# Optimization experiments

Hardware: AMD Instinct MI355X
Metric: run time of the kernel (lower is better)

## Reference

```python
import jax, jax.numpy as jnp
import numpy as np

N = 768                       # atoms
E = N * (N - 1)               # complete directed graph edges
DIM = 64                      # hidden dim
CUT = 5.0                     # rbf high
NC = 50                       # n_centers = ceil(5/0.1)
ODIM = 1                      # output_dim
NCONV = 3
_centers_np = np.linspace(0.0, CUT, NC)
CENTERS = jnp.asarray(_centers_np, jnp.float32)
GAP = float(_centers_np[1] - _centers_np[0])
RO_IN = 2 * ODIM + NC         # readout input: 2*output_dim + rbf fan_out = 52


def softplus_bt(x, beta, thr):
    # torch.nn.Softplus(beta, threshold): linear above threshold
    bx = beta * x
    return jnp.where(bx > thr, x, jax.nn.softplus(bx) / beta)


def rbf(d):
    # exp(-(1/gap) * (d - mu_k)^2); d: (..., 1) -> (..., NC)
    return jnp.exp((-1.0 / GAP) * (d - CENTERS) ** 2)


def setup_inputs() -> dict:
    key = jax.random.key(0)
    ks = jax.random.split(key, 24)
    atom_types = jax.random.randint(ks[0], (N,), 0, 100)
    edge_distances = jax.random.uniform(ks[1], (E, 1), jnp.float32) * CUT
    # complete directed graph, edge order matches the nested i,j loop (i!=j)
    ii = np.repeat(np.arange(N), N)
    jj = np.tile(np.arange(N), N)
    m = ii != jj
    src = jnp.asarray(ii[m], jnp.int32)
    dst = jnp.asarray(jj[m], jnp.int32)

    def p(k, shape, fan):
        return jax.random.normal(k, shape, jnp.float32) / np.sqrt(fan)

    embedding = p(ks[2], (100, DIM), DIM).at[0].set(0.0)  # padding_idx=0
    L = NCONV
    return {
        'atom_types': atom_types, 'edge_distances': edge_distances,
        'src': src, 'dst': dst, 'embedding': embedding,
        'w1': p(ks[3], (L, DIM, DIM), DIM),                 # node_layer1 (no bias)
        'pw1': p(ks[4], (L, NC, DIM), NC), 'pb1': p(ks[5], (L, DIM), NC),
        'pw2': p(ks[6], (L, DIM, DIM), DIM), 'pb2': p(ks[7], (L, DIM), DIM),
        'qw1': p(ks[8], (L, DIM, DIM), DIM), 'qb1': p(ks[9], (L, DIM), DIM),
        'qw2': p(ks[10], (L, DIM, DIM), DIM), 'qb2': p(ks[11], (L, DIM), DIM),
        'au_w1': p(ks[12], (DIM, 64), DIM), 'au_b1': p(ks[13], (64,), DIM),
        'au_w2': p(ks[14], (64, ODIM), 64), 'au_b2': p(ks[15], (ODIM,), 64),
        'ro_w1': p(ks[16], (RO_IN, 64), RO_IN), 'ro_b1': p(ks[17], (64,), RO_IN),
        'ro_w2': p(ks[18], (64, 2), 64), 'ro_b2': p(ks[19], (2,), 64),
    }


def reference(atom_types, edge_distances, src, dst, embedding,
              w1, pw1, pb1, pw2, pb2, qw1, qb1, qw2, qb2,
              au_w1, au_b1, au_w2, au_b2, ro_w1, ro_b1, ro_w2, ro_b2):
    h = embedding[atom_types]                       # (N, DIM)
    rbf_out = rbf(edge_distances)                   # (E, NC)
    for l in range(NCONV):
        nw = h @ w1[l]                              # node weights (N, DIM)
        e = softplus_bt(rbf_out @ pw1[l] + pb1[l], 0.5, 14) @ pw2[l] + pb2[l]  # (E, DIM)
        msg = nw[src] * e                           # gather-mul (E, DIM)
        agg = jax.ops.segment_sum(msg, dst, num_segments=N)  # scatter-sum (N, DIM)
        upd = softplus_bt(agg @ qw1[l] + qb1[l], 0.5, 14) @ qw2[l] + qb2[l]
        h = h + upd
    # atom_update with ShiftSoftplus (beta=1, shift=2, threshold=20)
    ha = softplus_bt(h @ au_w1 + au_b1, 1.0, 20) - jnp.log(jnp.float32(2.0))
    ha = ha @ au_w2 + au_b2                         # (N, ODIM)
    # readout over all ordered pairs i!=j, in edge order == (src, dst)
    edge_feat = jnp.concatenate([ha[src], ha[dst], rbf_out], axis=-1)  # (E, 52)
    logits = jax.nn.relu(edge_feat @ ro_w1 + ro_b1) @ ro_w2 + ro_b2    # (E, 2)
    return jax.nn.softmax(logits, axis=-1)
```

## Files before the change

kernel.cpp:

```cpp
#include <hip/hip_runtime.h>
#include <hip/hip_fp16.h>

#define NATOMS 768
#define NM1    767
#define NEDGE  (768*767)
#define DIM    64
#define NC     50
#define GAPF   (5.0f/49.0f)
#define NIGAP  (-49.0f/5.0f)
#define G      512
#define STEPF  (5.0f/511.0f)
#define INVSTEP (511.0f/5.0f)
#define LN2F   0.693147180559945f

#define WS_H     0
#define WS_NWA   49152
#define WS_NWB   73728
#define WS_HA    98304
#define WS_DISTT 99328
#define WS_TT    689152

__device__ __forceinline__ float softplus05(float x) {
    float bx = 0.5f * x;
    return (bx > 14.0f) ? x : 2.0f * __logf(1.0f + __expf(bx));
}
__device__ __forceinline__ int lane_bcast_i(int v, int l) {
    return __builtin_amdgcn_readlane(v, l);
}
__device__ __forceinline__ float lane_bcast_f(float v, int l) {
    return __uint_as_float((unsigned)__builtin_amdgcn_readlane((int)__float_as_uint(v), l));
}
__device__ __forceinline__ float2 pair2f(unsigned p) {
    __half2 h = *reinterpret_cast<__half2*>(&p);
    return __half22float2(h);
}

__global__ __launch_bounds__(256)
void k_pre(const int* __restrict__ types, const float* __restrict__ dist,
           const float* __restrict__ emb, const float* __restrict__ w1all,
           const float* __restrict__ pw1, const float* __restrict__ pb1,
           const float* __restrict__ pw2, const float* __restrict__ pb2,
           const float* __restrict__ row1, const float* __restrict__ rob1,
           float* __restrict__ ws) {
    __shared__ float s_t[4 * 64];
    __shared__ float s_tile[64][65];
    const int tid = threadIdx.x, widx = tid >> 6, c = tid & 63;
    float*  h     = ws + WS_H;
    __half* nwh   = (__half*)(ws + WS_NWA);
    float*  distT = ws + WS_DISTT;
    __half* TTh   = (__half*)(ws + WS_TT);
    const int b = blockIdx.x;

    if (b < 512) {
        const int w = b * 4 + widx, tbl = w >> 9, g = w & 511;
        const float d = g * STEPF;
        float val;
        if (tbl < 3) {
            const float* W1 = pw1 + tbl * NC * DIM;
            float t1 = pb1[tbl * DIM + c];
            for (int k = 0; k < NC; ++k) {
                float x = d - GAPF * (float)k;
                t1 = fmaf(__expf(NIGAP * x * x), W1[k * DIM + c], t1);
            }
            s_t[widx * 64 + c] = softplus05(t1);
            const float* W2 = pw2 + tbl * DIM * DIM;
            val = pb2[tbl * DIM + c];
            #pragma unroll 8
            for (int k = 0; k < DIM; ++k)
                val = fmaf(s_t[widx * 64 + k], W2[k * DIM + c], val);
        } else {
            val = rob1[c];
            for (int k = 0; k < NC; ++k) {
                float x = d - GAPF * (float)k;
                val = fmaf(__expf(NIGAP * x * x), row1[(2 + k) * DIM + c], val);
            }
        }
        __half* TTt = TTh + tbl * (G * DIM * 2);
        TTt[(g * DIM + c) * 2] = __float2half(val);
        if (g > 0) TTt[((g - 1) * DIM + c) * 2 + 1] = __float2half(val);
    } else if (b < 704) {
        const int i = (b - 512) * 4 + widx;
        float hv = emb[types[i] * DIM + c];
        h[i * DIM + c] = hv;
        s_t[widx * 64 + c] = hv;
        float acc = 0.0f;
        #pragma unroll 8
        for (int k = 0; k < DIM; ++k)
            acc = fmaf(s_t[widx * 64 + k], w1all[k * DIM + c], acc);
        nwh[(i >> 1) * 128 + c * 2 + (i & 1)] = __float2half(acc);
    } else {
        const int t = b - 704;
        const int I0 = (t / 12) * 64, J0 = (t % 12) * 64;
        #pragma unroll 4
        for (int r = 0; r < 16; ++r) {
            const int i = I0 + widx * 16 + r;
            const int j = J0 + c;
            s_tile[widx * 16 + r][c] =
                (i == j) ? 0.0f : dist[i * NM1 + (j - (j > i))];
        }
        __syncthreads();
        #pragma unroll 4
        for (int r = 0; r < 16; ++r) {
            const int j = J0 + widx * 16 + r;
            const int i = I0 + c;
            distT[j * NATOMS + i] = s_tile[c][widx * 16 + r];
        }
    }
}

__global__ __launch_bounds__(512)
void k_edgeupd(const __half2* __restrict__ TTl, const float* __restrict__ distT,
               const __half2* __restrict__ nwin,
               const float* __restrict__ qw1, const float* __restrict__ qb1,
               const float* __restrict__ qw2, const float* __restrict__ qb2,
               float* __restrict__ h,
               const float* __restrict__ wnext, __half* __restrict__ nwout,
               const float* __restrict__ auw1, const float* __restrict__ aub1,
               const float* __restrict__ auw2, const float* __restrict__ aub2,
               float* __restrict__ ha, int last) {
    __shared__ float s_part[8][64];
    __shared__ float s_upd[192];
    const int tid = threadIdx.x, widx = tid >> 6, c = tid & 63;
    const int j = blockIdx.x;
    const int s0 = widx * 96;

    const char* TTb = (const char*)TTl + c * 4;
    float csum = 0.0f;
    {
        float d = distT[j * NATOMS + s0 + c];
        float pos = d * INVSTEP;
        int g = (int)pos;
        g = (g < 0) ? 0 : ((g > 510) ? 510 : g);
        float f = pos - (float)g;
        int kx = g * 256;
        const char* nwrow = (const char*)(nwin + (s0 >> 1) * 64 + c);
        for (int grp = 0; grp < 4; ++grp) {
            unsigned sa[8], sb[8], sn[8];
            #pragma unroll
            for (int u = 0; u < 8; ++u) {
                const int t = grp * 8 + u;
                int kx0 = lane_bcast_i(kx, 2 * t);
                int kx1 = lane_bcast_i(kx, 2 * t + 1);
                sa[u] = *(const unsigned*)(TTb + kx0);
                sb[u] = *(const unsigned*)(TTb + kx1);
                sn[u] = *(const unsigned*)(nwrow + t * 256);
            }
            #pragma unroll
            for (int u = 0; u < 8; ++u) {
                const int t = grp * 8 + u;
                float f0 = lane_bcast_f(f, 2 * t);
                float f1 = lane_bcast_f(f, 2 * t + 1);
                float2 ta = pair2f(sa[u]);
                float2 tb = pair2f(sb[u]);
                float2 nwf = pair2f(sn[u]);
                float e0 = fmaf(f0, ta.y - ta.x, ta.x);
                float e1 = fmaf(f1, tb.y - tb.x, tb.x);
                csum = fmaf(e0, nwf.x, csum);
                csum = fmaf(e1, nwf.y, csum);
            }
        }
    }
    {
        float d = distT[j * NATOMS + s0 + 64 + (c & 31)];
        float pos = d * INVSTEP;
        int g = (int)pos;
        g = (g < 0) ? 0 : ((g > 510) ? 510 : g);
        float f = pos - (float)g;
        int kx = g * 256;
        const char* nwrow = (const char*)(nwin + ((s0 + 64) >> 1) * 64 + c);
        for (int grp = 0; grp < 2; ++grp) {
            unsigned sa[8], sb[8], sn[8];
            #pragma unroll
            for (int u = 0; u < 8; ++u) {
                const int t = grp * 8 + u;
                int kx0 = lane_bcast_i(kx, 2 * t);
                int kx1 = lane_bcast_i(kx, 2 * t + 1);
                sa[u] = *(const unsigned*)(TTb + kx0);
                sb[u] = *(const unsigned*)(TTb + kx1);
                sn[u] = *(const unsigned*)(nwrow + t * 256);
            }
            #pragma unroll
            for (int u = 0; u < 8; ++u) {
                const int t = grp * 8 + u;
                float f0 = lane_bcast_f(f, 2 * t);
                float f1 = lane_bcast_f(f, 2 * t + 1);
                float2 ta = pair2f(sa[u]);
                float2 tb = pair2f(sb[u]);
                float2 nwf = pair2f(sn[u]);
                float e0 = fmaf(f0, ta.y - ta.x, ta.x);
                float e1 = fmaf(f1, tb.y - tb.x, tb.x);
                csum = fmaf(e0, nwf.x, csum);
                csum = fmaf(e1, nwf.y, csum);
            }
        }
    }
    s_part[widx][c] = csum;
    __syncthreads();

    if (widx == 0) {
        float tot = 0.0f;
        #pragma unroll
        for (int w8 = 0; w8 < 8; ++w8) tot += s_part[w8][c];
        float2 t0 = __half22float2(*(const __half2*)TTb);
        float nwj = __half2float(((const __half*)nwin)[(j >> 1) * 128 + c * 2 + (j & 1)]);
        tot -= t0.x * nwj;
        s_upd[c] = tot;
        float t = qb1[c];
        #pragma unroll 8
        for (int k = 0; k < DIM; ++k) t = fmaf(s_upd[k], qw1[k * DIM + c], t);
        s_upd[64 + c] = softplus05(t);
        float o = qb2[c];
        #pragma unroll 8
        for (int k = 0; k < DIM; ++k) o = fmaf(s_upd[64 + k], qw2[k * DIM + c], o);
        float hn = h[j * DIM + c] + o;
        h[j * DIM + c] = hn;
        s_upd[128 + c] = hn;
        if (!last) {
            float v = 0.0f;
            #pragma unroll 8
            for (int k = 0; k < DIM; ++k) v = fmaf(s_upd[128 + k], wnext[k * DIM + c], v);
            nwout[(j >> 1) * 128 + c * 2 + (j & 1)] = __float2half(v);
        } else {
            float t2 = aub1[c];
            #pragma unroll 8
            for (int k = 0; k < DIM; ++k) t2 = fmaf(s_upd[128 + k], auw1[k * DIM + c], t2);
            t2 = ((t2 > 20.0f) ? t2 : __logf(1.0f + __expf(t2))) - LN2F;
            float v = t2 * auw2[c];
            #pragma unroll
            for (int s = 32; s > 0; s >>= 1) v += __shfl_down(v, s, 64);
            if (c == 0) ha[j] = v + aub2[0];
        }
    }
}

__global__ __launch_bounds__(256)
void k_ro(const float* __restrict__ dist, const int* __restrict__ src,
          const int* __restrict__ dst, const float* __restrict__ ha,
          const __half2* __restrict__ TTro,
          const float* __restrict__ row1, const float* __restrict__ row2,
          const float* __restrict__ rob2, float* __restrict__ out) {
    __shared__ float s_h[4][16 * 65];
    __shared__ float s_w2[128];
    const int tid = threadIdx.x, widx = tid >> 6, c = tid & 63;
    if (tid < 128) s_w2[tid] = row2[tid];
    __syncthreads();
    const int ebase = (blockIdx.x * 4 + widx) * 64;

    int kxv; float ff, fa, fb;
    {
        int eg = ebase + c;
        float d = dist[eg];
        float pos = d * INVSTEP;
        int kk = (int)pos;
        kk = (kk < 0) ? 0 : ((kk > 510) ? 510 : kk);
        kxv = kk * 256;
        ff = pos - (float)kk;
        fa = ha[src[eg]];
        fb = ha[dst[eg]];
    }
    const char* TTb2 = (const char*)TTro + c * 4;
    const float wa = row1[c], wb = row1[DIM + c];
    const int e2 = (c >> 1) & 15, p2 = c & 1, kh = c >> 5;
    const float bias2 = (kh == 0) ? rob2[p2] : 0.0f;
    float* sh = s_h[widx];
    #pragma unroll
    for (int ch = 0; ch < 4; ++ch) {
        #pragma unroll
        for (int half = 0; half < 2; ++half) {
            unsigned st[8];
            #pragma unroll
            for (int u = 0; u < 8; ++u) {
                const int le = ch * 16 + half * 8 + u;
                int kxu = lane_bcast_i(kxv, le);
                st[u] = *(const unsigned*)(TTb2 + kxu);
            }
            #pragma unroll
            for (int u = 0; u < 8; ++u) {
                const int le = ch * 16 + half * 8 + u;
                const int e = half * 8 + u;
                float fu  = lane_bcast_f(ff, le);
                float fau = lane_bcast_f(fa, le);
                float fbu = lane_bcast_f(fb, le);
                float2 tt = pair2f(st[u]);
                float hv = fmaf(fu, tt.y - tt.x, tt.x);
                hv = fmaf(fau, wa, hv);
                hv = fmaf(fbu, wb, hv);
                sh[e * 65 + c] = fmaxf(hv, 0.0f);
            }
        }
        float lsum = bias2;
        #pragma unroll 8
        for (int k8 = 0; k8 < 32; ++k8) {
            int k = kh * 32 + k8;
            lsum = fmaf(sh[e2 * 65 + k], s_w2[2 * k + p2], lsum);
        }
        lsum += __shfl_xor(lsum, 32, 64);
        float other = __shfl_xor(lsum, 1, 64);
        float m = fmaxf(lsum, other);
        float ea = __expf(lsum - m), eb = __expf(other - m);
        float r = ea / (ea + eb);
        if (c < 32) out[ebase * 2 + ch * 32 + c] = r;
    }
}

extern "C" void kernel_launch(void* const* d_in, const int* in_sizes, int n_in,
                              void* d_out, int out_size, void* d_ws, size_t ws_size,
                              hipStream_t stream) {
    const int*   types = (const int*)d_in[0];
    const float* dist  = (const float*)d_in[1];
    const int*   srcI  = (const int*)d_in[2];
    const int*   dstI  = (const int*)d_in[3];
    const float* emb   = (const float*)d_in[4];
    const float* w1    = (const float*)d_in[5];
    const float* pw1   = (const float*)d_in[6];
    const float* pb1   = (const float*)d_in[7];
    const float* pw2   = (const float*)d_in[8];
    const float* pb2   = (const float*)d_in[9];
    const float* qw1   = (const float*)d_in[10];
    const float* qb1   = (const float*)d_in[11];
    const float* qw2   = (const float*)d_in[12];
    const float* qb2   = (const float*)d_in[13];
    const float* auw1  = (const float*)d_in[14];
    const float* aub1  = (const float*)d_in[15];
    const float* auw2  = (const float*)d_in[16];
    const float* aub2  = (const float*)d_in[17];
    const float* row1  = (const float*)d_in[18];
    const float* rob1  = (const float*)d_in[19];
    const float* row2  = (const float*)d_in[20];
    const float* rob2  = (const float*)d_in[21];

    float* ws   = (float*)d_ws;
    float* outp = (float*)d_out;
    const __half2* TT = (const __half2*)(ws + WS_TT);
    __half2* nwbuf[2] = { (__half2*)(ws + WS_NWA), (__half2*)(ws + WS_NWB) };

    k_pre<<<848, 256, 0, stream>>>(types, dist, emb, w1, pw1, pb1, pw2, pb2,
                                   row1, rob1, ws);
    for (int l = 0; l < 3; ++l) {
        k_edgeupd<<<768, 512, 0, stream>>>(TT + l * (G * DIM),
            ws + WS_DISTT, nwbuf[l & 1],
            qw1 + l * DIM * DIM, qb1 + l * DIM,
            qw2 + l * DIM * DIM, qb2 + l * DIM,
            ws + WS_H,
            (l < 2) ? (w1 + (l + 1) * DIM * DIM) : w1, (__half*)nwbuf[(l + 1) & 1],
            auw1, aub1, auw2, aub2, ws + WS_HA, (l == 2) ? 1 : 0);
    }
    k_ro<<<2301, 256, 0, stream>>>(dist, srcI, dstI, ws + WS_HA, TT + 3 * (G * DIM),
                                   row1, row2, rob2, outp);
}
```

Baseline: 182.3 us.

## Fuse preprocessing and conv layers into one persistent kernel with grid barriers

Merges the preprocessing kernel and the three per-layer edge-update kernels into a single 768-block kernel, separated by a hierarchical atomic grid barrier in place of kernel launch boundaries. The distance transpose is rewritten as a plain strided copy instead of a shared-memory tiled transpose. The readout kernel now computes the src/dst atom indices arithmetically from the edge id instead of loading them from the index arrays. The aim is to cut launch overhead and tail gaps between the four kernels. In exchange it depends on all 768 blocks being co-resident, which the launch-bounds hint of six blocks per CU is meant to allow, and it adds a memset launch to reset the barrier.

```diff
diff --git a/kernel.cpp b/kernel.cpp
--- a/kernel.cpp
+++ b/kernel.cpp
@@ -19,6 +19,7 @@
 #define WS_HA    98304
 #define WS_DISTT 99328
 #define WS_TT    689152
+#define WS_BAR   820224
 
 __device__ __forceinline__ float softplus05(float x) {
     float bx = 0.5f * x;
@@ -35,207 +36,233 @@
     return __half22float2(h);
 }
 
-__global__ __launch_bounds__(256)
-void k_pre(const int* __restrict__ types, const float* __restrict__ dist,
-           const float* __restrict__ emb, const float* __restrict__ w1all,
+__device__ __forceinline__ void gbar(int* bar, int blk) {
+    __syncthreads();
+    if (threadIdx.x == 0) {
+        __threadfence();
+        int* root = bar;
+        int* gen  = bar + 16;
+        int* l1   = bar + 32 + (blk & 63) * 16;
+        int g = __hip_atomic_load(gen, __ATOMIC_RELAXED, __HIP_MEMORY_SCOPE_AGENT);
+        int a = __hip_atomic_fetch_add(l1, 1, __ATOMIC_ACQ_REL, __HIP_MEMORY_SCOPE_AGENT);
+        if (a == 11) {
+            __hip_atomic_store(l1, 0, __ATOMIC_RELAXED, __HIP_MEMORY_SCOPE_AGENT);
+            int r = __hip_atomic_fetch_add(root, 1, __ATOMIC_ACQ_REL, __HIP_MEMORY_SCOPE_AGENT);
+            if (r == 63) {
+                __hip_atomic_store(root, 0, __ATOMIC_RELAXED, __HIP_MEMORY_SCOPE_AGENT);
+                __hip_atomic_fetch_add(gen, 1, __ATOMIC_RELEASE, __HIP_MEMORY_SCOPE_AGENT);
+            } else {
+                while (__hip_atomic_load(gen, __ATOMIC_ACQUIRE, __HIP_MEMORY_SCOPE_AGENT) == g)
+                    __builtin_amdgcn_s_sleep(2);
+            }
+        } else {
+            while (__hip_atomic_load(gen, __ATOMIC_ACQUIRE, __HIP_MEMORY_SCOPE_AGENT) == g)
+                __builtin_amdgcn_s_sleep(2);
+        }
+        __threadfence();
+    }
+    __syncthreads();
+}
+
+__global__ __launch_bounds__(512, 6)
+void k_net(const int* __restrict__ types, const float* __restrict__ dist,
+           const float* __restrict__ emb, const float* __restrict__ w1,
            const float* __restrict__ pw1, const float* __restrict__ pb1,
            const float* __restrict__ pw2, const float* __restrict__ pb2,
+           const float* __restrict__ qw1, const float* __restrict__ qb1,
+           const float* __restrict__ qw2, const float* __restrict__ qb2,
+           const float* __restrict__ auw1, const float* __restrict__ aub1,
+           const float* __restrict__ auw2, const float* __restrict__ aub2,
            const float* __restrict__ row1, const float* __restrict__ rob1,
            float* __restrict__ ws) {
-    __shared__ float s_t[4 * 64];
-    __shared__ float s_tile[64][65];
-    const int tid = threadIdx.x, widx = tid >> 6, c = tid & 63;
-    float*  h     = ws + WS_H;
-    __half* nwh   = (__half*)(ws + WS_NWA);
-    float*  distT = ws + WS_DISTT;
-    __half* TTh   = (__half*)(ws + WS_TT);
-    const int b = blockIdx.x;
-
-    if (b < 512) {
-        const int w = b * 4 + widx, tbl = w >> 9, g = w & 511;
-        const float d = g * STEPF;
-        float val;
-        if (tbl < 3) {
-            const float* W1 = pw1 + tbl * NC * DIM;
-            float t1 = pb1[tbl * DIM + c];
-            for (int k = 0; k < NC; ++k) {
-                float x = d - GAPF * (float)k;
-                t1 = fmaf(__expf(NIGAP * x * x), W1[k * DIM + c], t1);
-            }
-            s_t[widx * 64 + c] = softplus05(t1);
-            const float* W2 = pw2 + tbl * DIM * DIM;
-            val = pb2[tbl * DIM + c];
-            #pragma unroll 8
-            for (int k = 0; k < DIM; ++k)
-                val = fmaf(s_t[widx * 64 + k], W2[k * DIM + c], val);
-        } else {
-            val = rob1[c];
-            for (int k = 0; k < NC; ++k) {
-                float x = d - GAPF * (float)k;
-                val = fmaf(__expf(NIGAP * x * x), row1[(2 + k) * DIM + c], val);
-            }
-        }
-        __half* TTt = TTh + tbl * (G * DIM * 2);
-        TTt[(g * DIM + c) * 2] = __float2half(val);
-        if (g > 0) TTt[((g - 1) * DIM + c) * 2 + 1] = __float2half(val);
-    } else if (b < 704) {
-        const int i = (b - 512) * 4 + widx;
-        float hv = emb[types[i] * DIM + c];
-        h[i * DIM + c] = hv;
-        s_t[widx * 64 + c] = hv;
-        float acc = 0.0f;
-        #pragma unroll 8
-        for (int k = 0; k < DIM; ++k)
-            acc = fmaf(s_t[widx * 64 + k], w1all[k * DIM + c], acc);
-        nwh[(i >> 1) * 128 + c * 2 + (i & 1)] = __float2half(acc);
-    } else {
-        const int t = b - 704;
-        const int I0 = (t / 12) * 64, J0 = (t % 12) * 64;
-        #pragma unroll 4
-        for (int r = 0; r < 16; ++r) {
-            const int i = I0 + widx * 16 + r;
-            const int j = J0 + c;
-            s_tile[widx * 16 + r][c] =
-                (i == j) ? 0.0f : dist[i * NM1 + (j - (j > i))];
-        }
-        __syncthreads();
-        #pragma unroll 4
-        for (int r = 0; r < 16; ++r) {
-            const int j = J0 + widx * 16 + r;
-            const int i = I0 + c;
-            distT[j * NATOMS + i] = s_tile[c][widx * 16 + r];
-        }
-    }
-}
-
-__global__ __launch_bounds__(512)
-void k_edgeupd(const __half2* __restrict__ TTl, const float* __restrict__ distT,
-               const __half2* __restrict__ nwin,
-               const float* __restrict__ qw1, const float* __restrict__ qb1,
-               const float* __restrict__ qw2, const float* __restrict__ qb2,
-               float* __restrict__ h,
-               const float* __restrict__ wnext, __half* __restrict__ nwout,
-               const float* __restrict__ auw1, const float* __restrict__ aub1,
-               const float* __restrict__ auw2, const float* __restrict__ aub2,
-               float* __restrict__ ha, int last) {
+    __shared__ float s_t[8][64];
     __shared__ float s_part[8][64];
     __shared__ float s_upd[192];
     const int tid = threadIdx.x, widx = tid >> 6, c = tid & 63;
-    const int j = blockIdx.x;
+    const int blk = blockIdx.x;
+    int* bar = (int*)(ws + WS_BAR);
+
+    float*   h     = ws + WS_H;
+    float*   haV   = ws + WS_HA;
+    float*   distT = ws + WS_DISTT;
+    __half*  TTh   = (__half*)(ws + WS_TT);
+    const __half2* TT = (const __half2*)(ws + WS_TT);
+    __half2* nwb[2] = { (__half2*)(ws + WS_NWA), (__half2*)(ws + WS_NWB) };
+
+    {
+        const int W = blk * 8 + widx;
+        if (W < 2048) {
+            const int tbl = W >> 9, g = W & 511;
+            const float d = g * STEPF;
+            float val;
+            if (tbl < 3) {
+                const float* W1 = pw1 + tbl * NC * DIM;
+                float t1 = pb1[tbl * DIM + c];
+                for (int k = 0; k < NC; ++k) {
+                    float x = d - GAPF * (float)k;
+                    t1 = fmaf(__expf(NIGAP * x * x), W1[k * DIM + c], t1);
+                }
+                s_t[widx][c] = softplus05(t1);
+                const float* W2 = pw2 + tbl * DIM * DIM;
+                val = pb2[tbl * DIM + c];
+                #pragma unroll 8
+                for (int k = 0; k < DIM; ++k)
+                    val = fmaf(s_t[widx][k], W2[k * DIM + c], val);
+            } else {
+                val = rob1[c];
+                for (int k = 0; k < NC; ++k) {
+                    float x = d - GAPF * (float)k;
+                    val = fmaf(__expf(NIGAP * x * x), row1[(2 + k) * DIM + c], val);
+                }
+            }
+            __half* TTt = TTh + tbl * (G * DIM * 2);
+            TTt[(g * DIM + c) * 2] = __float2half(val);
+            if (g > 0) TTt[((g - 1) * DIM + c) * 2 + 1] = __float2half(val);
+        } else if (W < 2816) {
+            const int i = W - 2048;
+            float hv = emb[types[i] * DIM + c];
+            h[i * DIM + c] = hv;
+            s_t[widx][c] = hv;
+            float acc = 0.0f;
+            #pragma unroll 8
+            for (int k = 0; k < DIM; ++k)
+                acc = fmaf(s_t[widx][k], w1[k * DIM + c], acc);
+            ((__half*)nwb[0])[(i >> 1) * 128 + c * 2 + (i & 1)] = __float2half(acc);
+        } else if (W < 3392) {
+            const int u = W - 2816;
+            for (int t = 0; t < 16; ++t) {
+                const int idx = u * 1024 + t * 64 + c;
+                const int jj = idx / NATOMS, ii = idx - jj * NATOMS;
+                distT[idx] = (ii == jj) ? 0.0f : dist[ii * NM1 + (jj - (jj > ii))];
+            }
+        }
+    }
+    gbar(bar, blk);
+
+    const int j = blk;
     const int s0 = widx * 96;
-
-    const char* TTb = (const char*)TTl + c * 4;
-    float csum = 0.0f;
-    {
-        float d = distT[j * NATOMS + s0 + c];
-        float pos = d * INVSTEP;
-        int g = (int)pos;
-        g = (g < 0) ? 0 : ((g > 510) ? 510 : g);
-        float f = pos - (float)g;
-        int kx = g * 256;
-        const char* nwrow = (const char*)(nwin + (s0 >> 1) * 64 + c);
-        for (int grp = 0; grp < 4; ++grp) {
-            unsigned sa[8], sb[8], sn[8];
+    for (int l = 0; l < 3; ++l) {
+        const __half2* TTl   = TT + l * (G * DIM);
+        const __half2* nwin  = nwb[l & 1];
+        __half*        nwout = (__half*)nwb[(l + 1) & 1];
+        const float* qw1l = qw1 + l * DIM * DIM; const float* qb1l = qb1 + l * DIM;
+        const float* qw2l = qw2 + l * DIM * DIM; const float* qb2l = qb2 + l * DIM;
+        const float* wnx  = (l < 2) ? (w1 + (l + 1) * DIM * DIM) : w1;
+        const int last = (l == 2);
+
+        const char* TTb = (const char*)TTl + c * 4;
+        float csum = 0.0f;
+        {
+            float d = distT[j * NATOMS + s0 + c];
+            float pos = d * INVSTEP;
+            int g = (int)pos;
+            g = (g < 0) ? 0 : ((g > 510) ? 510 : g);
+            float f = pos - (float)g;
+            int kx = g * 256;
+            const char* nwrow = (const char*)(nwin + (s0 >> 1) * 64 + c);
+            for (int grp = 0; grp < 4; ++grp) {
+                unsigned sa[8], sb[8], sn[8];
+                #pragma unroll
+                for (int u = 0; u < 8; ++u) {
+                    const int t = grp * 8 + u;
+                    int kx0 = lane_bcast_i(kx, 2 * t);
+                    int kx1 = lane_bcast_i(kx, 2 * t + 1);
+                    sa[u] = *(const unsigned*)(TTb + kx0);
+                    sb[u] = *(const unsigned*)(TTb + kx1);
+                    sn[u] = *(const unsigned*)(nwrow + t * 256);
+                }
+                #pragma unroll
+                for (int u = 0; u < 8; ++u) {
+                    const int t = grp * 8 + u;
+                    float f0 = lane_bcast_f(f, 2 * t);
+                    float f1 = lane_bcast_f(f, 2 * t + 1);
+                    float2 ta = pair2f(sa[u]);
+                    float2 tb = pair2f(sb[u]);
+                    float2 nwf = pair2f(sn[u]);
+                    float e0 = fmaf(f0, ta.y - ta.x, ta.x);
+                    float e1 = fmaf(f1, tb.y - tb.x, tb.x);
+                    csum = fmaf(e0, nwf.x, csum);
+                    csum = fmaf(e1, nwf.y, csum);
+                }
+            }
+        }
+        {
+            float d = distT[j * NATOMS + s0 + 64 + (c & 31)];
+            float pos = d * INVSTEP;
+            int g = (int)pos;
+            g = (g < 0) ? 0 : ((g > 510) ? 510 : g);
+            float f = pos - (float)g;
+            int kx = g * 256;
+            const char* nwrow = (const char*)(nwin + ((s0 + 64) >> 1) * 64 + c);
+            for (int grp = 0; grp < 2; ++grp) {
+                unsigned sa[8], sb[8], sn[8];
+                #pragma unroll
+                for (int u = 0; u < 8; ++u) {
+                    const int t = grp * 8 + u;
+                    int kx0 = lane_bcast_i(kx, 2 * t);
+                    int kx1 = lane_bcast_i(kx, 2 * t + 1);
+                    sa[u] = *(const unsigned*)(TTb + kx0);
+                    sb[u] = *(const unsigned*)(TTb + kx1);
+                    sn[u] = *(const unsigned*)(nwrow + t * 256);
+                }
+                #pragma unroll
+                for (int u = 0; u < 8; ++u) {
+                    const int t = grp * 8 + u;
+                    float f0 = lane_bcast_f(f, 2 * t);
+                    float f1 = lane_bcast_f(f, 2 * t + 1);
+                    float2 ta = pair2f(sa[u]);
+                    float2 tb = pair2f(sb[u]);
+                    float2 nwf = pair2f(sn[u]);
+                    float e0 = fmaf(f0, ta.y - ta.x, ta.x);
+                    float e1 = fmaf(f1, tb.y - tb.x, tb.x);
+                    csum = fmaf(e0, nwf.x, csum);
+                    csum = fmaf(e1, nwf.y, csum);
+                }
+            }
+        }
+        s_part[widx][c] = csum;
+        __syncthreads();
+
+        if (widx == 0) {
+            float tot = 0.0f;
             #pragma unroll
-            for (int u = 0; u < 8; ++u) {
-                const int t = grp * 8 + u;
-                int kx0 = lane_bcast_i(kx, 2 * t);
-                int kx1 = lane_bcast_i(kx, 2 * t + 1);
-                sa[u] = *(const unsigned*)(TTb + kx0);
-                sb[u] = *(const unsigned*)(TTb + kx1);
-                sn[u] = *(const unsigned*)(nwrow + t * 256);
-            }
-            #pragma unroll
-            for (int u = 0; u < 8; ++u) {
-                const int t = grp * 8 + u;
-                float f0 = lane_bcast_f(f, 2 * t);
-                float f1 = lane_bcast_f(f, 2 * t + 1);
-                float2 ta = pair2f(sa[u]);
-                float2 tb = pair2f(sb[u]);
-                float2 nwf = pair2f(sn[u]);
-                float e0 = fmaf(f0, ta.y - ta.x, ta.x);
-                float e1 = fmaf(f1, tb.y - tb.x, tb.x);
-                csum = fmaf(e0, nwf.x, csum);
-                csum = fmaf(e1, nwf.y, csum);
-            }
-        }
-    }
-    {
-        float d = distT[j * NATOMS + s0 + 64 + (c & 31)];
-        float pos = d * INVSTEP;
-        int g = (int)pos;
-        g = (g < 0) ? 0 : ((g > 510) ? 510 : g);
-        float f = pos - (float)g;
-        int kx = g * 256;
-        const char* nwrow = (const char*)(nwin + ((s0 + 64) >> 1) * 64 + c);
-        for (int grp = 0; grp < 2; ++grp) {
-            unsigned sa[8], sb[8], sn[8];
-            #pragma unroll
-            for (int u = 0; u < 8; ++u) {
-                const int t = grp * 8 + u;
-                int kx0 = lane_bcast_i(kx, 2 * t);
-                int kx1 = lane_bcast_i(kx, 2 * t + 1);
-                sa[u] = *(const unsigned*)(TTb + kx0);
-                sb[u] = *(const unsigned*)(TTb + kx1);
-                sn[u] = *(const unsigned*)(nwrow + t * 256);
-            }
-            #pragma unroll
-            for (int u = 0; u < 8; ++u) {
-                const int t = grp * 8 + u;
-                float f0 = lane_bcast_f(f, 2 * t);
-                float f1 = lane_bcast_f(f, 2 * t + 1);
-                float2 ta = pair2f(sa[u]);
-                float2 tb = pair2f(sb[u]);
-                float2 nwf = pair2f(sn[u]);
-                float e0 = fmaf(f0, ta.y - ta.x, ta.x);
-                float e1 = fmaf(f1, tb.y - tb.x, tb.x);
-                csum = fmaf(e0, nwf.x, csum);
-                csum = fmaf(e1, nwf.y, csum);
-            }
-        }
-    }
-    s_part[widx][c] = csum;
-    __syncthreads();
-
-    if (widx == 0) {
-        float tot = 0.0f;
-        #pragma unroll
-        for (int w8 = 0; w8 < 8; ++w8) tot += s_part[w8][c];
-        float2 t0 = __half22float2(*(const __half2*)TTb);
-        float nwj = __half2float(((const __half*)nwin)[(j >> 1) * 128 + c * 2 + (j & 1)]);
-        tot -= t0.x * nwj;
-        s_upd[c] = tot;
-        float t = qb1[c];
-        #pragma unroll 8
-        for (int k = 0; k < DIM; ++k) t = fmaf(s_upd[k], qw1[k * DIM + c], t);
-        s_upd[64 + c] = softplus05(t);
-        float o = qb2[c];
-        #pragma unroll 8
-        for (int k = 0; k < DIM; ++k) o = fmaf(s_upd[64 + k], qw2[k * DIM + c], o);
-        float hn = h[j * DIM + c] + o;
-        h[j * DIM + c] = hn;
-        s_upd[128 + c] = hn;
-        if (!last) {
-            float v = 0.0f;
+            for (int w8 = 0; w8 < 8; ++w8) tot += s_part[w8][c];
+            float2 t0 = __half22float2(*(const __half2*)TTb);
+            float nwj = __half2float(((const __half*)nwin)[(j >> 1) * 128 + c * 2 + (j & 1)]);
+            tot -= t0.x * nwj;
+            s_upd[c] = tot;
+            float t = qb1l[c];
             #pragma unroll 8
-            for (int k = 0; k < DIM; ++k) v = fmaf(s_upd[128 + k], wnext[k * DIM + c], v);
-            nwout[(j >> 1) * 128 + c * 2 + (j & 1)] = __float2half(v);
-        } else {
-            float t2 = aub1[c];
+            for (int k = 0; k < DIM; ++k) t = fmaf(s_upd[k], qw1l[k * DIM + c], t);
+            s_upd[64 + c] = softplus05(t);
+            float o = qb2l[c];
             #pragma unroll 8
-            for (int k = 0; k < DIM; ++k) t2 = fmaf(s_upd[128 + k], auw1[k * DIM + c], t2);
-            t2 = ((t2 > 20.0f) ? t2 : __logf(1.0f + __expf(t2))) - LN2F;
-            float v = t2 * auw2[c];
-            #pragma unroll
-            for (int s = 32; s > 0; s >>= 1) v += __shfl_down(v, s, 64);
-            if (c == 0) ha[j] = v + aub2[0];
-        }
+            for (int k = 0; k < DIM; ++k) o = fmaf(s_upd[64 + k], qw2l[k * DIM + c], o);
+            float hn = h[j * DIM + c] + o;
+            h[j * DIM + c] = hn;
+            s_upd[128 + c] = hn;
+            if (!last) {
+                float v = 0.0f;
+                #pragma unroll 8
+                for (int k = 0; k < DIM; ++k) v = fmaf(s_upd[128 + k], wnx[k * DIM + c], v);
+                nwout[(j >> 1) * 128 + c * 2 + (j & 1)] = __float2half(v);
+            } else {
+                float t2 = aub1[c];
+                #pragma unroll 8
+                for (int k = 0; k < DIM; ++k) t2 = fmaf(s_upd[128 + k], auw1[k * DIM + c], t2);
+                t2 = ((t2 > 20.0f) ? t2 : __logf(1.0f + __expf(t2))) - LN2F;
+                float v = t2 * auw2[c];
+                #pragma unroll
+                for (int s = 32; s > 0; s >>= 1) v += __shfl_down(v, s, 64);
+                if (c == 0) haV[j] = v + aub2[0];
+            }
+        }
+        if (!last) gbar(bar, blk);
     }
 }
 
 __global__ __launch_bounds__(256)
-void k_ro(const float* __restrict__ dist, const int* __restrict__ src,
-          const int* __restrict__ dst, const float* __restrict__ ha,
+void k_ro(const float* __restrict__ dist, const float* __restrict__ ha,
           const __half2* __restrict__ TTro,
           const float* __restrict__ row1, const float* __restrict__ row2,
           const float* __restrict__ rob2, float* __restrict__ out) {
@@ -255,8 +282,11 @@
         kk = (kk < 0) ? 0 : ((kk > 510) ? 510 : kk);
         kxv = kk * 256;
         ff = pos - (float)kk;
-        fa = ha[src[eg]];
-        fb = ha[dst[eg]];
+        unsigned i = (unsigned)(((unsigned long long)(unsigned)eg * 2867044662ull) >> 41);
+        int r = eg - (int)i * 767;
+        int jd = r + (r >= (int)i);
+        fa = ha[i];
+        fb = ha[jd];
     }
     const char* TTb2 = (const char*)TTro + c * 4;
     const float wa = row1[c], wb = row1[DIM + c];
@@ -308,8 +338,6 @@
                               hipStream_t stream) {
     const int*   types = (const int*)d_in[0];
     const float* dist  = (const float*)d_in[1];
-    const int*   srcI  = (const int*)d_in[2];
-    const int*   dstI  = (const int*)d_in[3];
     const float* emb   = (const float*)d_in[4];
     const float* w1    = (const float*)d_in[5];
     const float* pw1   = (const float*)d_in[6];
@@ -332,19 +360,11 @@
     float* ws   = (float*)d_ws;
     float* outp = (float*)d_out;
     const __half2* TT = (const __half2*)(ws + WS_TT);
-    __half2* nwbuf[2] = { (__half2*)(ws + WS_NWA), (__half2*)(ws + WS_NWB) };
-
-    k_pre<<<848, 256, 0, stream>>>(types, dist, emb, w1, pw1, pb1, pw2, pb2,
+
+    hipMemsetAsync(ws + WS_BAR, 0, 1056 * sizeof(int), stream);
+    k_net<<<768, 512, 0, stream>>>(types, dist, emb, w1, pw1, pb1, pw2, pb2,
+                                   qw1, qb1, qw2, qb2, auw1, aub1, auw2, aub2,
                                    row1, rob1, ws);
-    for (int l = 0; l < 3; ++l) {
-        k_edgeupd<<<768, 512, 0, stream>>>(TT + l * (G * DIM),
-            ws + WS_DISTT, nwbuf[l & 1],
-            qw1 + l * DIM * DIM, qb1 + l * DIM,
-            qw2 + l * DIM * DIM, qb2 + l * DIM,
-            ws + WS_H,
-            (l < 2) ? (w1 + (l + 1) * DIM * DIM) : w1, (__half*)nwbuf[(l + 1) & 1],
-            auw1, aub1, auw2, aub2, ws + WS_HA, (l == 2) ? 1 : 0);
-    }
-    k_ro<<<2301, 256, 0, stream>>>(dist, srcI, dstI, ws + WS_HA, TT + 3 * (G * DIM),
+    k_ro<<<2301, 256, 0, stream>>>(dist, ws + WS_HA, TT + 3 * (G * DIM),
                                    row1, row2, rob2, outp);
 }
```

Measured after the change: 639.5 us. 251% more time.

## Split conv aggregation across three blocks per atom with last-block reduction

Applied to the files above, without the earlier changes.

The per-atom aggregation kernel now runs three 256-thread blocks per destination atom instead of one 512-thread block. Each block writes a partial sum to a workspace buffer, and an atomic counter picks the last block to finish the reduction and the node MLP. This raises grid size and occupancy, and removes the odd half-wave tail segment. Separately, the readout kernel derives the src/dst indices arithmetically from the edge index instead of loading the index arrays. The cost is extra global traffic, threadfences, atomics and a memset per launch.

```diff
diff --git a/kernel.cpp b/kernel.cpp
--- a/kernel.cpp
+++ b/kernel.cpp
@@ -19,6 +19,8 @@
 #define WS_HA    98304
 #define WS_DISTT 99328
 #define WS_TT    689152
+#define WS_PART  820224
+#define WS_CNT   967680
 
 __device__ __forceinline__ float softplus05(float x) {
     float bx = 0.5f * x;
@@ -108,42 +110,45 @@
     }
 }
 
-__global__ __launch_bounds__(512)
-void k_edgeupd(const __half2* __restrict__ TTl, const float* __restrict__ distT,
-               const __half2* __restrict__ nwin,
-               const float* __restrict__ qw1, const float* __restrict__ qb1,
-               const float* __restrict__ qw2, const float* __restrict__ qb2,
-               float* __restrict__ h,
-               const float* __restrict__ wnext, __half* __restrict__ nwout,
-               const float* __restrict__ auw1, const float* __restrict__ aub1,
-               const float* __restrict__ auw2, const float* __restrict__ aub2,
-               float* __restrict__ ha, int last) {
-    __shared__ float s_part[8][64];
+__global__ __launch_bounds__(256, 8)
+void k_conv(const __half2* __restrict__ TTl, const float* __restrict__ distT,
+            const __half2* __restrict__ nwin,
+            const float* __restrict__ qw1, const float* __restrict__ qb1,
+            const float* __restrict__ qw2, const float* __restrict__ qb2,
+            float* __restrict__ h,
+            const float* __restrict__ wnext, __half* __restrict__ nwout,
+            const float* __restrict__ auw1, const float* __restrict__ aub1,
+            const float* __restrict__ auw2, const float* __restrict__ aub2,
+            float* __restrict__ ha, float* __restrict__ pbuf, int* __restrict__ cnt,
+            int last) {
+    __shared__ float s_part[4][64];
     __shared__ float s_upd[192];
+    __shared__ int s_flag;
     const int tid = threadIdx.x, widx = tid >> 6, c = tid & 63;
-    const int j = blockIdx.x;
-    const int s0 = widx * 96;
+    const int b = blockIdx.x;
+    const int j = b / 3, seg = b - j * 3;
+    const int sb = seg * 256 + widx * 64;
 
     const char* TTb = (const char*)TTl + c * 4;
     float csum = 0.0f;
     {
-        float d = distT[j * NATOMS + s0 + c];
+        float d = distT[j * NATOMS + sb + c];
         float pos = d * INVSTEP;
         int g = (int)pos;
         g = (g < 0) ? 0 : ((g > 510) ? 510 : g);
         float f = pos - (float)g;
         int kx = g * 256;
-        const char* nwrow = (const char*)(nwin + (s0 >> 1) * 64 + c);
+        const char* nwrow = (const char*)(nwin + (sb >> 1) * 64 + c);
         for (int grp = 0; grp < 4; ++grp) {
-            unsigned sa[8], sb[8], sn[8];
+            unsigned sa[8], sb8[8], sn[8];
             #pragma unroll
             for (int u = 0; u < 8; ++u) {
                 const int t = grp * 8 + u;
                 int kx0 = lane_bcast_i(kx, 2 * t);
                 int kx1 = lane_bcast_i(kx, 2 * t + 1);
-                sa[u] = *(const unsigned*)(TTb + kx0);
-                sb[u] = *(const unsigned*)(TTb + kx1);
-                sn[u] = *(const unsigned*)(nwrow + t * 256);
+                sa[u]  = *(const unsigned*)(TTb + kx0);
+                sb8[u] = *(const unsigned*)(TTb + kx1);
+                sn[u]  = *(const unsigned*)(nwrow + t * 256);
             }
             #pragma unroll
             for (int u = 0; u < 8; ++u) {
@@ -151,7 +156,7 @@
                 float f0 = lane_bcast_f(f, 2 * t);
                 float f1 = lane_bcast_f(f, 2 * t + 1);
                 float2 ta = pair2f(sa[u]);
-                float2 tb = pair2f(sb[u]);
+                float2 tb = pair2f(sb8[u]);
                 float2 nwf = pair2f(sn[u]);
                 float e0 = fmaf(f0, ta.y - ta.x, ta.x);
                 float e1 = fmaf(f1, tb.y - tb.x, tb.x);
@@ -160,47 +165,27 @@
             }
         }
     }
-    {
-        float d = distT[j * NATOMS + s0 + 64 + (c & 31)];
-        float pos = d * INVSTEP;
-        int g = (int)pos;
-        g = (g < 0) ? 0 : ((g > 510) ? 510 : g);
-        float f = pos - (float)g;
-        int kx = g * 256;
-        const char* nwrow = (const char*)(nwin + ((s0 + 64) >> 1) * 64 + c);
-        for (int grp = 0; grp < 2; ++grp) {
-            unsigned sa[8], sb[8], sn[8];
-            #pragma unroll
-            for (int u = 0; u < 8; ++u) {
-                const int t = grp * 8 + u;
-                int kx0 = lane_bcast_i(kx, 2 * t);
-                int kx1 = lane_bcast_i(kx, 2 * t + 1);
-                sa[u] = *(const unsigned*)(TTb + kx0);
-                sb[u] = *(const unsigned*)(TTb + kx1);
-                sn[u] = *(const unsigned*)(nwrow + t * 256);
-            }
-            #pragma unroll
-            for (int u = 0; u < 8; ++u) {
-                const int t = grp * 8 + u;
-                float f0 = lane_bcast_f(f, 2 * t);
-                float f1 = lane_bcast_f(f, 2 * t + 1);
-                float2 ta = pair2f(sa[u]);
-                float2 tb = pair2f(sb[u]);
-                float2 nwf = pair2f(sn[u]);
-                float e0 = fmaf(f0, ta.y - ta.x, ta.x);
-                float e1 = fmaf(f1, tb.y - tb.x, tb.x);
-                csum = fmaf(e0, nwf.x, csum);
-                csum = fmaf(e1, nwf.y, csum);
-            }
-        }
-    }
     s_part[widx][c] = csum;
     __syncthreads();
 
     if (widx == 0) {
-        float tot = 0.0f;
-        #pragma unroll
-        for (int w8 = 0; w8 < 8; ++w8) tot += s_part[w8][c];
+        float p = s_part[0][c] + s_part[1][c] + s_part[2][c] + s_part[3][c];
+        pbuf[(j * 3 + seg) * 64 + c] = p;
+        __threadfence();
+    }
+    __syncthreads();
+    if (tid == 0) {
+        int old = atomicAdd(&cnt[j], 1);
+        s_flag = (old == 2);
+    }
+    __syncthreads();
+    if (!s_flag) return;
+
+    if (widx == 0) {
+        __threadfence();
+        float tot = pbuf[(j * 3 + 0) * 64 + c]
+                  + pbuf[(j * 3 + 1) * 64 + c]
+                  + pbuf[(j * 3 + 2) * 64 + c];
         float2 t0 = __half22float2(*(const __half2*)TTb);
         float nwj = __half2float(((const __half*)nwin)[(j >> 1) * 128 + c * 2 + (j & 1)]);
         tot -= t0.x * nwj;
@@ -230,12 +215,12 @@
             for (int s = 32; s > 0; s >>= 1) v += __shfl_down(v, s, 64);
             if (c == 0) ha[j] = v + aub2[0];
         }
+        if (c == 0) cnt[j] = 0;
     }
 }
 
 __global__ __launch_bounds__(256)
-void k_ro(const float* __restrict__ dist, const int* __restrict__ src,
-          const int* __restrict__ dst, const float* __restrict__ ha,
+void k_ro(const float* __restrict__ dist, const float* __restrict__ ha,
           const __half2* __restrict__ TTro,
           const float* __restrict__ row1, const float* __restrict__ row2,
           const float* __restrict__ rob2, float* __restrict__ out) {
@@ -255,8 +240,11 @@
         kk = (kk < 0) ? 0 : ((kk > 510) ? 510 : kk);
         kxv = kk * 256;
         ff = pos - (float)kk;
-        fa = ha[src[eg]];
-        fb = ha[dst[eg]];
+        unsigned i = (unsigned)(((unsigned long long)(unsigned)eg * 2867044662ull) >> 41);
+        int r = eg - (int)i * 767;
+        int jd = r + (r >= (int)i);
+        fa = ha[i];
+        fb = ha[jd];
     }
     const char* TTb2 = (const char*)TTro + c * 4;
     const float wa = row1[c], wb = row1[DIM + c];
@@ -308,8 +296,6 @@
                               hipStream_t stream) {
     const int*   types = (const int*)d_in[0];
     const float* dist  = (const float*)d_in[1];
-    const int*   srcI  = (const int*)d_in[2];
-    const int*   dstI  = (const int*)d_in[3];
     const float* emb   = (const float*)d_in[4];
     const float* w1    = (const float*)d_in[5];
     const float* pw1   = (const float*)d_in[6];
@@ -333,18 +319,21 @@
     float* outp = (float*)d_out;
     const __half2* TT = (const __half2*)(ws + WS_TT);
     __half2* nwbuf[2] = { (__half2*)(ws + WS_NWA), (__half2*)(ws + WS_NWB) };
-
+    float* pbuf = ws + WS_PART;
+    int*   cnt  = (int*)(ws + WS_CNT);
+
+    hipMemsetAsync(cnt, 0, 768 * sizeof(int), stream);
     k_pre<<<848, 256, 0, stream>>>(types, dist, emb, w1, pw1, pb1, pw2, pb2,
                                    row1, rob1, ws);
     for (int l = 0; l < 3; ++l) {
-        k_edgeupd<<<768, 512, 0, stream>>>(TT + l * (G * DIM),
+        k_conv<<<2304, 256, 0, stream>>>(TT + l * (G * DIM),
             ws + WS_DISTT, nwbuf[l & 1],
             qw1 + l * DIM * DIM, qb1 + l * DIM,
             qw2 + l * DIM * DIM, qb2 + l * DIM,
             ws + WS_H,
             (l < 2) ? (w1 + (l + 1) * DIM * DIM) : w1, (__half*)nwbuf[(l + 1) & 1],
-            auw1, aub1, auw2, aub2, ws + WS_HA, (l == 2) ? 1 : 0);
-    }
-    k_ro<<<2301, 256, 0, stream>>>(dist, srcI, dstI, ws + WS_HA, TT + 3 * (G * DIM),
+            auw1, aub1, auw2, aub2, ws + WS_HA, pbuf, cnt, (l == 2) ? 1 : 0);
+    }
+    k_ro<<<2301, 256, 0, stream>>>(dist, ws + WS_HA, TT + 3 * (G * DIM),
                                    row1, row2, rob2, outp);
 }
```

Measured after the change: 397.9 us. 118% more time.

## Split lanes across source halves with 8-byte table loads; compute src/dst analytically

Applied to the files above, without the earlier changes.

The node-weight buffer becomes a plain row-major half array. In the edge-update kernel, each half-wavefront now handles one of the two interleaved sources, using a single 8-byte table load that covers two channels instead of two 4-byte loads. The two halves are combined with a cross-lane shuffle before the shared-memory reduction. The readout kernel stops loading src/dst indices and derives them from the edge id with a magic-number division, which relies on the fixed complete-graph edge ordering.

```diff
diff --git a/kernel.cpp b/kernel.cpp
--- a/kernel.cpp
+++ b/kernel.cpp
@@ -87,7 +87,7 @@
         #pragma unroll 8
         for (int k = 0; k < DIM; ++k)
             acc = fmaf(s_t[widx * 64 + k], w1all[k * DIM + c], acc);
-        nwh[(i >> 1) * 128 + c * 2 + (i & 1)] = __float2half(acc);
+        nwh[i * 64 + c] = __float2half(acc);
     } else {
         const int t = b - 704;
         const int I0 = (t / 12) * 64, J0 = (t % 12) * 64;
@@ -110,7 +110,7 @@
 
 __global__ __launch_bounds__(512)
 void k_edgeupd(const __half2* __restrict__ TTl, const float* __restrict__ distT,
-               const __half2* __restrict__ nwin,
+               const __half* __restrict__ nwin,
                const float* __restrict__ qw1, const float* __restrict__ qb1,
                const float* __restrict__ qw2, const float* __restrict__ qb2,
                float* __restrict__ h,
@@ -123,9 +123,10 @@
     const int tid = threadIdx.x, widx = tid >> 6, c = tid & 63;
     const int j = blockIdx.x;
     const int s0 = widx * 96;
-
-    const char* TTb = (const char*)TTl + c * 4;
-    float csum = 0.0f;
+    const int half = c >> 5, cl = c & 31;
+
+    const char* TTrow = (const char*)TTl + cl * 8;
+    float2 csum = make_float2(0.0f, 0.0f);
     {
         float d = distT[j * NATOMS + s0 + c];
         float pos = d * INVSTEP;
@@ -133,16 +134,16 @@
         g = (g < 0) ? 0 : ((g > 510) ? 510 : g);
         float f = pos - (float)g;
         int kx = g * 256;
-        const char* nwrow = (const char*)(nwin + (s0 >> 1) * 64 + c);
+        const char* nwrow = (const char*)nwin + s0 * 128 + half * 128 + cl * 4;
         for (int grp = 0; grp < 4; ++grp) {
-            unsigned sa[8], sb[8], sn[8];
+            uint2 st[8]; unsigned sn[8];
             #pragma unroll
             for (int u = 0; u < 8; ++u) {
                 const int t = grp * 8 + u;
                 int kx0 = lane_bcast_i(kx, 2 * t);
                 int kx1 = lane_bcast_i(kx, 2 * t + 1);
-                sa[u] = *(const unsigned*)(TTb + kx0);
-                sb[u] = *(const unsigned*)(TTb + kx1);
+                int kxs = half ? kx1 : kx0;
+                st[u] = *(const uint2*)(TTrow + kxs);
                 sn[u] = *(const unsigned*)(nwrow + t * 256);
             }
             #pragma unroll
@@ -150,33 +151,34 @@
                 const int t = grp * 8 + u;
                 float f0 = lane_bcast_f(f, 2 * t);
                 float f1 = lane_bcast_f(f, 2 * t + 1);
-                float2 ta = pair2f(sa[u]);
-                float2 tb = pair2f(sb[u]);
+                float fs = half ? f1 : f0;
+                float2 ta = pair2f(st[u].x);
+                float2 tb = pair2f(st[u].y);
                 float2 nwf = pair2f(sn[u]);
-                float e0 = fmaf(f0, ta.y - ta.x, ta.x);
-                float e1 = fmaf(f1, tb.y - tb.x, tb.x);
-                csum = fmaf(e0, nwf.x, csum);
-                csum = fmaf(e1, nwf.y, csum);
+                float e0 = fmaf(fs, ta.y - ta.x, ta.x);
+                float e1 = fmaf(fs, tb.y - tb.x, tb.x);
+                csum.x = fmaf(e0, nwf.x, csum.x);
+                csum.y = fmaf(e1, nwf.y, csum.y);
             }
         }
     }
     {
-        float d = distT[j * NATOMS + s0 + 64 + (c & 31)];
+        float d = distT[j * NATOMS + s0 + 64 + cl];
         float pos = d * INVSTEP;
         int g = (int)pos;
         g = (g < 0) ? 0 : ((g > 510) ? 510 : g);
         float f = pos - (float)g;
         int kx = g * 256;
-        const char* nwrow = (const char*)(nwin + ((s0 + 64) >> 1) * 64 + c);
+        const char* nwrow = (const char*)nwin + (s0 + 64) * 128 + half * 128 + cl * 4;
         for (int grp = 0; grp < 2; ++grp) {
-            unsigned sa[8], sb[8], sn[8];
+            uint2 st[8]; unsigned sn[8];
             #pragma unroll
             for (int u = 0; u < 8; ++u) {
                 const int t = grp * 8 + u;
                 int kx0 = lane_bcast_i(kx, 2 * t);
                 int kx1 = lane_bcast_i(kx, 2 * t + 1);
-                sa[u] = *(const unsigned*)(TTb + kx0);
-                sb[u] = *(const unsigned*)(TTb + kx1);
+                int kxs = half ? kx1 : kx0;
+                st[u] = *(const uint2*)(TTrow + kxs);
                 sn[u] = *(const unsigned*)(nwrow + t * 256);
             }
             #pragma unroll
@@ -184,25 +186,29 @@
                 const int t = grp * 8 + u;
                 float f0 = lane_bcast_f(f, 2 * t);
                 float f1 = lane_bcast_f(f, 2 * t + 1);
-                float2 ta = pair2f(sa[u]);
-                float2 tb = pair2f(sb[u]);
+                float fs = half ? f1 : f0;
+                float2 ta = pair2f(st[u].x);
+                float2 tb = pair2f(st[u].y);
                 float2 nwf = pair2f(sn[u]);
-                float e0 = fmaf(f0, ta.y - ta.x, ta.x);
-                float e1 = fmaf(f1, tb.y - tb.x, tb.x);
-                csum = fmaf(e0, nwf.x, csum);
-                csum = fmaf(e1, nwf.y, csum);
-            }
-        }
-    }
-    s_part[widx][c] = csum;
+                float e0 = fmaf(fs, ta.y - ta.x, ta.x);
+                float e1 = fmaf(fs, tb.y - tb.x, tb.x);
+                csum.x = fmaf(e0, nwf.x, csum.x);
+                csum.y = fmaf(e1, nwf.y, csum.y);
+            }
+        }
+    }
+    float2 tot2;
+    tot2.x = csum.x + __shfl_xor(csum.x, 32, 64);
+    tot2.y = csum.y + __shfl_xor(csum.y, 32, 64);
+    if (half == 0) *(float2*)&s_part[widx][2 * cl] = tot2;
     __syncthreads();
 
     if (widx == 0) {
         float tot = 0.0f;
         #pragma unroll
         for (int w8 = 0; w8 < 8; ++w8) tot += s_part[w8][c];
-        float2 t0 = __half22float2(*(const __half2*)TTb);
-        float nwj = __half2float(((const __half*)nwin)[(j >> 1) * 128 + c * 2 + (j & 1)]);
+        float2 t0 = pair2f(((const unsigned*)TTl)[c]);
+        float nwj = __half2float(nwin[j * 64 + c]);
         tot -= t0.x * nwj;
         s_upd[c] = tot;
         float t = qb1[c];
@@ -219,7 +225,7 @@
             float v = 0.0f;
             #pragma unroll 8
             for (int k = 0; k < DIM; ++k) v = fmaf(s_upd[128 + k], wnext[k * DIM + c], v);
-            nwout[(j >> 1) * 128 + c * 2 + (j & 1)] = __float2half(v);
+            nwout[j * 64 + c] = __float2half(v);
         } else {
             float t2 = aub1[c];
             #pragma unroll 8
@@ -234,8 +240,7 @@
 }
 
 __global__ __launch_bounds__(256)
-void k_ro(const float* __restrict__ dist, const int* __restrict__ src,
-          const int* __restrict__ dst, const float* __restrict__ ha,
+void k_ro(const float* __restrict__ dist, const float* __restrict__ ha,
           const __half2* __restrict__ TTro,
           const float* __restrict__ row1, const float* __restrict__ row2,
           const float* __restrict__ rob2, float* __restrict__ out) {
@@ -255,8 +260,11 @@
         kk = (kk < 0) ? 0 : ((kk > 510) ? 510 : kk);
         kxv = kk * 256;
         ff = pos - (float)kk;
-        fa = ha[src[eg]];
-        fb = ha[dst[eg]];
+        unsigned i = (unsigned)(((unsigned long long)(unsigned)eg * 2867044662ull) >> 41);
+        int r = eg - (int)i * 767;
+        int jd = r + (r >= (int)i);
+        fa = ha[i];
+        fb = ha[jd];
     }
     const char* TTb2 = (const char*)TTro + c * 4;
     const float wa = row1[c], wb = row1[DIM + c];
@@ -308,8 +316,6 @@
                               hipStream_t stream) {
     const int*   types = (const int*)d_in[0];
     const float* dist  = (const float*)d_in[1];
-    const int*   srcI  = (const int*)d_in[2];
-    const int*   dstI  = (const int*)d_in[3];
     const float* emb   = (const float*)d_in[4];
     const float* w1    = (const float*)d_in[5];
     const float* pw1   = (const float*)d_in[6];
@@ -332,7 +338,7 @@
     float* ws   = (float*)d_ws;
     float* outp = (float*)d_out;
     const __half2* TT = (const __half2*)(ws + WS_TT);
-    __half2* nwbuf[2] = { (__half2*)(ws + WS_NWA), (__half2*)(ws + WS_NWB) };
+    __half* nwbuf[2] = { (__half*)(ws + WS_NWA), (__half*)(ws + WS_NWB) };
 
     k_pre<<<848, 256, 0, stream>>>(types, dist, emb, w1, pw1, pb1, pw2, pb2,
                                    row1, rob1, ws);
@@ -342,9 +348,9 @@
             qw1 + l * DIM * DIM, qb1 + l * DIM,
             qw2 + l * DIM * DIM, qb2 + l * DIM,
             ws + WS_H,
-            (l < 2) ? (w1 + (l + 1) * DIM * DIM) : w1, (__half*)nwbuf[(l + 1) & 1],
+            (l < 2) ? (w1 + (l + 1) * DIM * DIM) : w1, nwbuf[(l + 1) & 1],
             auw1, aub1, auw2, aub2, ws + WS_HA, (l == 2) ? 1 : 0);
     }
-    k_ro<<<2301, 256, 0, stream>>>(dist, srcI, dstI, ws + WS_HA, TT + 3 * (G * DIM),
+    k_ro<<<2301, 256, 0, stream>>>(dist, ws + WS_HA, TT + 3 * (G * DIM),
                                    row1, row2, rob2, outp);
 }
```

New measurement: 181.2 us. About the same (-0.6%).
